# Optimization experiments

Measured on AMD Instinct MI355X. Metric: run time of the kernel, lower is better.

The kernel has to match this reference:

```python
import jax, jax.numpy as jnp
import numpy as np

HEAD_DIM = 64
N_HEADS = 64
N_KV = 8
Q_MULT = N_HEADS // N_KV  # 8
HIDDEN = 2880
SEQ = 1024
BATCH = 2
SLIDING_WINDOW = 128  # layer_idx=0 -> window active
ROPE_THETA = 150000.0
SCALING = 32.0
NTK_ALPHA = 1.0
NTK_BETA = 32.0
INIT_CTX = 4096
EPS = 1e-5


def _rope_caches(seq_len):
    # YaRN rotary caches (static numpy precompute, as in the source module)
    steps = np.arange(0, HEAD_DIM, 2, dtype=np.float32)
    freq = np.power(np.float32(ROPE_THETA), steps / np.float32(HEAD_DIM))
    concentration = np.float32(0.1) * np.log(np.float32(SCALING)) + 1.0
    d_half = np.float32(HEAD_DIM / 2.0)
    log_base = np.log(np.float32(ROPE_THETA))
    low = d_half * np.log(np.float32(INIT_CTX) / (np.float32(NTK_BETA) * np.float32(2.0 * np.pi))) / log_base
    high = d_half * np.log(np.float32(INIT_CTX) / (np.float32(NTK_ALPHA) * np.float32(2.0 * np.pi))) / log_base
    ramp = (np.arange(HEAD_DIM // 2, dtype=np.float32) - low) / (high - low)
    mask = 1.0 - np.clip(ramp, 0.0, 1.0)
    inv_freq = (1.0 / (np.float32(SCALING) * freq)) * (1.0 - mask) + (1.0 / freq) * mask
    pos = np.arange(seq_len, dtype=np.float32)
    freqs = np.einsum('i,j->ij', pos, inv_freq.astype(np.float32))
    cos = (np.cos(freqs) * concentration).astype(np.float32)
    sin = (np.sin(freqs) * concentration).astype(np.float32)
    return jnp.asarray(cos), jnp.asarray(sin)


def _apply_rotary(t, cos, sin):
    # t: (B, S, ..., head_dim); cos/sin: (S, head_dim//2). Rotate-half style.
    shape = (1, t.shape[1]) + (1,) * (t.ndim - 3) + (cos.shape[-1],)
    c = cos.reshape(shape)
    s = sin.reshape(shape)
    first, second = jnp.split(t, 2, axis=-1)
    return jnp.concatenate([first * c - second * s, second * c + first * s], axis=-1)


def setup_inputs() -> dict:
    key = jax.random.key(0)
    ks = jax.random.split(key, 6)
    qkv_dim = (N_HEADS + 2 * N_KV) * HEAD_DIM  # 5120
    return {
        'x': jax.random.normal(ks[0], (BATCH, SEQ, HIDDEN), dtype=jnp.float32),
        'norm_w': jnp.ones((HIDDEN,), dtype=jnp.float32),
        'qkv_w': jax.random.normal(ks[1], (qkv_dim, HIDDEN), dtype=jnp.float32) * 0.02,
        'qkv_b': jax.random.normal(ks[2], (qkv_dim,), dtype=jnp.float32) * 0.02,
        'out_w': jax.random.normal(ks[3], (HIDDEN, N_HEADS * HEAD_DIM), dtype=jnp.float32) * 0.02,
        'out_b': jax.random.normal(ks[4], (HIDDEN,), dtype=jnp.float32) * 0.02,
        'sinks': jax.random.normal(ks[5], (N_HEADS,), dtype=jnp.float32),
    }


def reference(x, norm_w, qkv_w, qkv_b, out_w, out_b, sinks):
    B, S, _ = x.shape
    # RMSNorm (fp32 accumulation)
    xf = x.astype(jnp.float32)
    rms = jnp.mean(xf * xf, axis=-1, keepdims=True)
    t = (xf * jax.lax.rsqrt(rms + EPS) * norm_w).astype(x.dtype)
    # QKV projection (fp32 accumulation)
    qkv = jnp.matmul(t.astype(jnp.float32), qkv_w.T) + qkv_b
    q_dim = N_HEADS * HEAD_DIM
    kv_dim = N_KV * HEAD_DIM
    q = qkv[..., :q_dim].reshape(B, S, N_KV, Q_MULT, HEAD_DIM)
    k = qkv[..., q_dim:q_dim + kv_dim].reshape(B, S, N_KV, HEAD_DIM)
    v = qkv[..., q_dim + kv_dim:].reshape(B, S, N_KV, HEAD_DIM)
    # YaRN rotary embedding
    cos, sin = _rope_caches(S)
    q = _apply_rotary(q, cos, sin)
    k = _apply_rotary(k, cos, sin)
    # causal + sliding-window mask
    neg_inf = jnp.float32(-jnp.inf)
    mask = jnp.triu(jnp.full((S, S), neg_inf, dtype=jnp.float32), k=1)
    mask = mask + jnp.tril(jnp.full((S, S), neg_inf, dtype=jnp.float32), k=-SLIDING_WINDOW)
    sm_scale = jnp.float32(1.0 / np.sqrt(HEAD_DIM))
    # GQA attention with sink logits
    logits = jnp.einsum('bqhmd,bkhd->bhmqk', q, k) * sm_scale + mask[None, None, None]
    sink = jnp.broadcast_to(sinks.reshape(1, N_KV, Q_MULT, 1, 1), (B, N_KV, Q_MULT, S, 1))
    logits = jnp.concatenate([logits, sink], axis=-1)
    w = jax.nn.softmax(logits, axis=-1)[..., :-1]  # drop sink column
    attn = jnp.einsum('bhmqk,bkhd->bqhmd', w, v).reshape(B, S, N_HEADS * HEAD_DIM)
    # output projection (fp32 accumulation) + residual
    out = jnp.matmul(attn, out_w.T) + out_b
    return x + out
```

## Files before the change

### kernel.cpp

```cpp
#include <hip/hip_runtime.h>

typedef unsigned short ushort_t;
typedef __attribute__((ext_vector_type(8))) short short8;
typedef __attribute__((ext_vector_type(8))) __bf16 bf16x8;
typedef __attribute__((ext_vector_type(4))) float float4v;
typedef __attribute__((ext_vector_type(4))) unsigned int uint4v;

__device__ __forceinline__ float bf2f(ushort_t u) {
    unsigned int v = ((unsigned int)u) << 16;
    return __builtin_bit_cast(float, v);
}
__device__ __forceinline__ ushort_t f2bf(float f) {
    unsigned int u = __builtin_bit_cast(unsigned int, f);
    unsigned int lsb = (u >> 16) & 1u;
    u += 0x7fffu + lsb;
    return (ushort_t)(u >> 16);
}
__device__ __forceinline__ uint4v pack8(const ushort_t* r) {
    uint4v u;
#pragma unroll
    for (int i = 0; i < 4; ++i)
        u[i] = (unsigned int)r[2 * i] | ((unsigned int)r[2 * i + 1] << 16);
    return u;
}
__device__ __forceinline__ void unpack8(uint4v u, float* f) {
#pragma unroll
    for (int i = 0; i < 4; ++i) {
        unsigned int x = u[i];
        f[2 * i] = __builtin_bit_cast(float, x << 16);
        f[2 * i + 1] = __builtin_bit_cast(float, x & 0xffff0000u);
    }
}
__device__ __forceinline__ uint4v ld8f32_bf(const float* p) {
    float4v a = *(const float4v*)p;
    float4v b = *(const float4v*)(p + 4);
    ushort_t r[8];
#pragma unroll
    for (int j = 0; j < 4; ++j) { r[j] = f2bf(a[j]); r[4 + j] = f2bf(b[j]); }
    return pack8(r);
}

#if __has_builtin(__builtin_amdgcn_global_load_lds)
#define HAVE_GLDS 1
__device__ __forceinline__ void glds16(const ushort_t* gp, ushort_t* lp) {
    __builtin_amdgcn_global_load_lds((const __attribute__((address_space(1))) void*)gp,
                                     (__attribute__((address_space(3))) void*)lp, 16, 0, 0);
}
#else
#define HAVE_GLDS 0
#endif

template <typename V>
__device__ __forceinline__ auto mfma_sel(V a, V b, float4v c, int)
    -> decltype(__builtin_amdgcn_mfma_f32_16x16x32_bf16(a, b, c, 0, 0, 0)) {
    return __builtin_amdgcn_mfma_f32_16x16x32_bf16(a, b, c, 0, 0, 0);
}
template <typename V>
__device__ __forceinline__ float4v mfma_sel(V a, V b, float4v c, long) {
    return __builtin_amdgcn_mfma_f32_16x16x32_bf16(__builtin_bit_cast(bf16x8, a),
                                                   __builtin_bit_cast(bf16x8, b), c, 0, 0, 0);
}
__device__ __forceinline__ float4v mfma_bf16(short8 a, short8 b, float4v c) {
    return mfma_sel(a, b, c, 0);
}

__device__ __forceinline__ float wave_sum(float v) {
#pragma unroll
    for (int o = 32; o; o >>= 1) v += __shfl_xor(v, o);
    return v;
}

#define HIDDEN 2880
#define NTOK 2048
#define QKV_DIM 5120
#define ATTN_DIM 4096
#define SM_SCALE 0.125f

__global__ __launch_bounds__(256) void f32_to_bf16_dual_kernel(const float* __restrict__ a,
                                                               ushort_t* __restrict__ ao, int na8,
                                                               const float* __restrict__ b,
                                                               ushort_t* __restrict__ bo, int nb8) {
    int idx = blockIdx.x * 256 + threadIdx.x;
    if (idx < na8) {
        *(uint4v*)(ao + (size_t)idx * 8) = ld8f32_bf(a + (size_t)idx * 8);
    } else {
        int j = idx - na8;
        if (j < nb8) *(uint4v*)(bo + (size_t)j * 8) = ld8f32_bf(b + (size_t)j * 8);
    }
}

__global__ __launch_bounds__(256) void rmsnorm_kernel(const float* __restrict__ x,
                                                      const float* __restrict__ wgt,
                                                      ushort_t* __restrict__ out) {
    const int tok = blockIdx.x, tid = threadIdx.x;
    const float* xr = x + (size_t)tok * HIDDEN;
    float v[16];
    float ss = 0.f;
#pragma unroll
    for (int i = 0; i < 2; ++i) {
        int c = tid + i * 256;
        if (c < 360) {
            float4v a = *(const float4v*)(xr + c * 8);
            float4v b = *(const float4v*)(xr + c * 8 + 4);
#pragma unroll
            for (int j = 0; j < 4; ++j) { v[i * 8 + j] = a[j]; v[i * 8 + 4 + j] = b[j]; }
#pragma unroll
            for (int j = 0; j < 8; ++j) ss += v[i * 8 + j] * v[i * 8 + j];
        }
    }
    ss = wave_sum(ss);
    __shared__ float red[4];
    if ((tid & 63) == 0) red[tid >> 6] = ss;
    __syncthreads();
    float scale = rsqrtf((red[0] + red[1] + red[2] + red[3]) * (1.f / 2880.f) + 1e-5f);
#pragma unroll
    for (int i = 0; i < 2; ++i) {
        int c = tid + i * 256;
        if (c < 360) {
            float4v wa = *(const float4v*)(wgt + c * 8);
            float4v wb = *(const float4v*)(wgt + c * 8 + 4);
            ushort_t r[8];
#pragma unroll
            for (int j = 0; j < 4; ++j) {
                r[j] = f2bf(v[i * 8 + j] * scale * wa[j]);
                r[4 + j] = f2bf(v[i * 8 + 4 + j] * scale * wb[j]);
            }
            *(uint4v*)(out + (size_t)tok * HIDDEN + c * 8) = pack8(r);
        }
    }
}

__global__ __launch_bounds__(256) void rope_apply_kernel(ushort_t* __restrict__ qkv) {
    int idx = blockIdx.x * 256 + threadIdx.x;
    int tok = idx / 288;
    int rem = idx - tok * 288;
    int h = rem >> 2, dg = rem & 3;
    int s = tok & 1023;
    size_t base = (size_t)tok * QKV_DIM + (h < 64 ? h * 64 : 4096 + (h - 64) * 64) + dg * 8;
    uint4v u1 = *(const uint4v*)(qkv + base);
    uint4v u2 = *(const uint4v*)(qkv + base + 32);
    float f1[8], f2[8];
    unpack8(u1, f1);
    unpack8(u2, f2);
    const float step = (float)(11.918390573078392 / 32.0);
    const float conc = (float)(1.3465735902799727);
    const float low = (float)(8.092890725542669);
    const float invden = (float)(1.0 / 9.305804387286162);
    ushort_t r1[8], r2[8];
#pragma unroll
    for (int jj = 0; jj < 8; ++jj) {
        int j = dg * 8 + jj;
        float invf = __expf(-(float)j * step);
        float ramp = ((float)j - low) * invden;
        float mask = 1.f - fminf(fmaxf(ramp, 0.f), 1.f);
        float inv_freq = invf * ((1.f - mask) * 0.03125f + mask);
        float ang = (float)s * inv_freq;
        float c = cosf(ang) * conc;
        float sn = sinf(ang) * conc;
        r1[jj] = f2bf(f1[jj] * c - f2[jj] * sn);
        r2[jj] = f2bf(f2[jj] * c + f1[jj] * sn);
    }
    *(uint4v*)(qkv + base) = pack8(r1);
    *(uint4v*)(qkv + base + 32) = pack8(r2);
}

template <int BN, bool RESID, bool OUTF32, bool BF16B>
__global__ __launch_bounds__(256) void gemm_kernel(const ushort_t* __restrict__ A,
                                                   const void* __restrict__ B,
                                                   const float* __restrict__ bias,
                                                   const float* __restrict__ resid,
                                                   void* __restrict__ Cout, int M, int N, int K) {
    constexpr int BM = 128, BK = 64;
    constexpr bool GL = BF16B && (HAVE_GLDS != 0);
    constexpr int LDT = GL ? 64 : 72;
    constexpr int NBUF = GL ? 2 : 1;
    static_assert(BN == 160 || BN == 128 || BN == 96 || BN == 64, "");
    __shared__ __align__(16) ushort_t As[NBUF][BM * LDT];
    __shared__ __align__(16) ushort_t Bs[NBUF][BN * LDT];

    const int m0 = blockIdx.y * BM;
    const int n0 = blockIdx.x * BN;
    const int tid = threadIdx.x;
    const int w = tid >> 6, lane = tid & 63;
    const int quad = lane >> 4, l16 = lane & 15;

    constexpr int WN = BN / 2;
    constexpr int NI = WN / 16;
    const int wm = (w >> 1) * 64;
    const int wn = (w & 1) * WN;

    float4v acc[4][NI];
#pragma unroll
    for (int i = 0; i < 4; ++i)
#pragma unroll
        for (int j = 0; j < NI; ++j) acc[i][j] = (float4v){0.f, 0.f, 0.f, 0.f};

    const int nk = K / BK;

#if HAVE_GLDS
    if constexpr (GL) {
        constexpr int NAI = BM / 32;
        constexpr int NBI = BN / 32;
        const ushort_t* Bp = (const ushort_t*)B;
        const ushort_t* agp[NAI];
        const ushort_t* bgp[NBI];
        ushort_t* alp[2][NAI];
        ushort_t* blp[2][NBI];
#pragma unroll
        for (int i = 0; i < NAI; ++i) {
            int sb = (w * NAI + i) * 64;
            int s = sb + lane, r = s >> 3, p = s & 7, c = p ^ (r & 7);
            agp[i] = A + (size_t)(m0 + r) * K + c * 8;
            alp[0][i] = &As[0][sb * 8];
            alp[1][i] = &As[1][sb * 8];
        }
#pragma unroll
        for (int i = 0; i < NBI; ++i) {
            int sb = (w * NBI + i) * 64;
            int s = sb + lane, r = s >> 3, p = s & 7, c = p ^ (r & 7);
            bgp[i] = Bp + (size_t)(n0 + r) * K + c * 8;
            blp[0][i] = &Bs[0][sb * 8];
            blp[1][i] = &Bs[1][sb * 8];
        }
#pragma unroll
        for (int i = 0; i < NAI; ++i) glds16(agp[i], alp[0][i]);
#pragma unroll
        for (int i = 0; i < NBI; ++i) glds16(bgp[i], blp[0][i]);
        __syncthreads();

        for (int kt = 0; kt < nk; ++kt) {
            const int cur = kt & 1;
            if (kt + 1 < nk) {
                const int k0 = (kt + 1) * BK;
#pragma unroll
                for (int i = 0; i < NAI; ++i) glds16(agp[i] + k0, alp[cur ^ 1][i]);
#pragma unroll
                for (int i = 0; i < NBI; ++i) glds16(bgp[i] + k0, blp[cur ^ 1][i]);
            }
            const ushort_t* Asb = As[cur];
            const ushort_t* Bsb = Bs[cur];
#pragma unroll
            for (int ks = 0; ks < 2; ++ks) {
                short8 af[4], bfr[NI];
#pragma unroll
                for (int mi = 0; mi < 4; ++mi) {
                    int row = wm + mi * 16 + l16;
                    af[mi] = *(const short8*)(Asb + row * LDT + ((ks * 4 + quad) ^ (row & 7)) * 8);
                }
#pragma unroll
                for (int ni = 0; ni < NI; ++ni) {
                    int row = wn + ni * 16 + l16;
                    bfr[ni] = *(const short8*)(Bsb + row * LDT + ((ks * 4 + quad) ^ (row & 7)) * 8);
                }
#pragma unroll
                for (int mi = 0; mi < 4; ++mi)
#pragma unroll
                    for (int ni = 0; ni < NI; ++ni)
                        acc[mi][ni] = mfma_bf16(af[mi], bfr[ni], acc[mi][ni]);
            }
            __syncthreads();
        }
    } else
#endif
    {
        constexpr int ACH = BM * BK / 8 / 256;
        constexpr int BCH = BN * BK / 8 / 256;
        uint4v areg[ACH], breg[BCH];
#pragma unroll
        for (int i = 0; i < ACH; ++i) {
            int c = tid + i * 256, r = c >> 3, col = c & 7;
            areg[i] = *(const uint4v*)(A + (size_t)(m0 + r) * K + col * 8);
        }
#pragma unroll
        for (int i = 0; i < BCH; ++i) {
            int c = tid + i * 256, r = c >> 3, col = c & 7;
            if constexpr (BF16B)
                breg[i] = *(const uint4v*)((const ushort_t*)B + (size_t)(n0 + r) * K + col * 8);
            else
                breg[i] = ld8f32_bf((const float*)B + (size_t)(n0 + r) * K + col * 8);
        }
        for (int kt = 0; kt < nk; ++kt) {
            __syncthreads();
#pragma unroll
            for (int i = 0; i < ACH; ++i) {
                int c = tid + i * 256, r = c >> 3, col = c & 7;
                *(uint4v*)(&As[0][r * LDT + col * 8]) = areg[i];
            }
#pragma unroll
            for (int i = 0; i < BCH; ++i) {
                int c = tid + i * 256, r = c >> 3, col = c & 7;
                *(uint4v*)(&Bs[0][r * LDT + col * 8]) = breg[i];
            }
            __syncthreads();
            if (kt + 1 < nk) {
                const int k0 = (kt + 1) * BK;
#pragma unroll
                for (int i = 0; i < ACH; ++i) {
                    int c = tid + i * 256, r = c >> 3, col = c & 7;
                    areg[i] = *(const uint4v*)(A + (size_t)(m0 + r) * K + k0 + col * 8);
                }
#pragma unroll
                for (int i = 0; i < BCH; ++i) {
                    int c = tid + i * 256, r = c >> 3, col = c & 7;
                    if constexpr (BF16B)
                        breg[i] = *(const uint4v*)((const ushort_t*)B + (size_t)(n0 + r) * K + k0 + col * 8);
                    else
                        breg[i] = ld8f32_bf((const float*)B + (size_t)(n0 + r) * K + k0 + col * 8);
                }
            }
#pragma unroll
            for (int ks = 0; ks < 2; ++ks) {
                short8 af[4], bfr[NI];
#pragma unroll
                for (int mi = 0; mi < 4; ++mi)
                    af[mi] = *(const short8*)(&As[0][(wm + mi * 16 + l16) * LDT + ks * 32 + quad * 8]);
#pragma unroll
                for (int ni = 0; ni < NI; ++ni)
                    bfr[ni] = *(const short8*)(&Bs[0][(wn + ni * 16 + l16) * LDT + ks * 32 + quad * 8]);
#pragma unroll
                for (int mi = 0; mi < 4; ++mi)
#pragma unroll
                    for (int ni = 0; ni < NI; ++ni)
                        acc[mi][ni] = mfma_bf16(af[mi], bfr[ni], acc[mi][ni]);
            }
        }
    }

#pragma unroll
    for (int ni = 0; ni < NI; ++ni) {
        int gc = n0 + wn + ni * 16 + l16;
        float bv = bias[gc];
#pragma unroll
        for (int mi = 0; mi < 4; ++mi) {
#pragma unroll
            for (int r = 0; r < 4; ++r) {
                int gr = m0 + wm + mi * 16 + quad * 4 + r;
                float vv = acc[mi][ni][r] + bv;
                if constexpr (RESID) vv += resid[(size_t)gr * N + gc];
                if constexpr (OUTF32) ((float*)Cout)[(size_t)gr * N + gc] = vv;
                else ((ushort_t*)Cout)[(size_t)gr * N + gc] = f2bf(vv);
            }
        }
    }
}

__global__ __launch_bounds__(256, 2) void attn_mfma_kernel(const ushort_t* __restrict__ qkv,
                                                           const float* __restrict__ sinks,
                                                           ushort_t* __restrict__ attnbuf) {
    constexpr int LDK = 72, LDV = 200, LDP = 200;
    __shared__ __align__(16) ushort_t Ks[192 * LDK];
    __shared__ __align__(16) ushort_t Vt[64 * LDV];
    __shared__ __align__(16) ushort_t Pb[4][16 * LDP];

    const int qc = blockIdx.x, kvh = blockIdx.y >> 1, half = blockIdx.y & 1, b = blockIdx.z;
    const int tid = threadIdx.x;
    const int w = tid >> 6, lane = tid & 63;
    const int quad = lane >> 4, l16 = lane & 15;
    const int w0 = qc * 64 - 127;

    for (int c = tid; c < 192 * 8; c += 256) {
        int row = c >> 3, col8 = c & 7;
        int pos = w0 + row;
        pos = pos < 0 ? 0 : (pos > 1023 ? 1023 : pos);
        size_t gk = ((size_t)(b * 1024 + pos)) * QKV_DIM + 4096 + kvh * 64 + col8 * 8;
        *(uint4v*)(Ks + row * LDK + col8 * 8) = *(const uint4v*)(qkv + gk);
        uint4v vv = *(const uint4v*)(qkv + gk + 512);
        ushort_t vs[8];
#pragma unroll
        for (int i = 0; i < 4; ++i) {
            vs[2 * i] = (ushort_t)(vv[i] & 0xffffu);
            vs[2 * i + 1] = (ushort_t)(vv[i] >> 16);
        }
#pragma unroll
        for (int j = 0; j < 8; ++j) Vt[(col8 * 8 + j) * LDV + row] = vs[j];
    }
    __syncthreads();

    short8 Vf[6][4];
#pragma unroll
    for (int kt = 0; kt < 6; ++kt)
#pragma unroll
        for (int nv = 0; nv < 4; ++nv)
            Vf[kt][nv] = *(const short8*)(Vt + (nv * 16 + l16) * LDV + kt * 32 + quad * 8);

    ushort_t* Pw = Pb[w];
    const int h = kvh * 8 + half * 4 + w;
    const float sink_f = sinks[h];

    for (int qtile = 0; qtile < 4; ++qtile) {
        const int tokb = b * 1024 + qc * 64 + qtile * 16;

        short8 qf[2];
        {
            const ushort_t* qp = qkv + ((size_t)(tokb + l16)) * QKV_DIM + h * 64 + quad * 8;
            qf[0] = *(const short8*)qp;
            qf[1] = *(const short8*)(qp + 32);
        }

        float4v acc[12];
#pragma unroll
        for (int nt = 0; nt < 12; ++nt) acc[nt] = (float4v){0.f, 0.f, 0.f, 0.f};
#pragma unroll
        for (int nt = 0; nt < 12; ++nt) {
#pragma unroll
            for (int ks = 0; ks < 2; ++ks) {
                short8 kf = *(const short8*)(Ks + (nt * 16 + l16) * LDK + ks * 32 + quad * 8);
                acc[nt] = mfma_bf16(qf[ks], kf, acc[nt]);
            }
        }

        float linv[4];
#pragma unroll
        for (int r = 0; r < 4; ++r) {
            const int ql = qtile * 16 + quad * 4 + r;
            float e[12];
            float mx = -1e30f;
#pragma unroll
            for (int nt = 0; nt < 12; ++nt) {
                int row_k = nt * 16 + l16;
                bool valid = (row_k >= ql) && (row_k <= ql + 127) && (w0 + row_k >= 0);
                float s = valid ? acc[nt][r] * SM_SCALE : -1e30f;
                e[nt] = s;
                mx = fmaxf(mx, s);
            }
#pragma unroll
            for (int o = 1; o < 16; o <<= 1) mx = fmaxf(mx, __shfl_xor(mx, o));
            float M = fmaxf(mx, sink_f);
            float ls = 0.f;
#pragma unroll
            for (int nt = 0; nt < 12; ++nt) {
                float ev = (e[nt] > -1e29f) ? __expf(e[nt] - M) : 0.f;
                e[nt] = ev;
                ls += ev;
            }
#pragma unroll
            for (int o = 1; o < 16; o <<= 1) ls += __shfl_xor(ls, o);
            linv[r] = 1.f / (ls + __expf(sink_f - M));
#pragma unroll
            for (int nt = 0; nt < 12; ++nt)
                Pw[(quad * 4 + r) * LDP + nt * 16 + l16] = f2bf(e[nt]);
        }

        float4v accO[4];
#pragma unroll
        for (int nv = 0; nv < 4; ++nv) accO[nv] = (float4v){0.f, 0.f, 0.f, 0.f};
#pragma unroll
        for (int kt = 0; kt < 6; ++kt) {
            short8 pf = *(const short8*)(Pw + l16 * LDP + kt * 32 + quad * 8);
#pragma unroll
            for (int nv = 0; nv < 4; ++nv) accO[nv] = mfma_bf16(pf, Vf[kt][nv], accO[nv]);
        }

#pragma unroll
        for (int r = 0; r < 4; ++r) {
            size_t ob = ((size_t)(tokb + quad * 4 + r)) * ATTN_DIM + h * 64 + l16;
#pragma unroll
            for (int nv = 0; nv < 4; ++nv)
                attnbuf[ob + nv * 16] = f2bf(accO[nv][r] * linv[r]);
        }
    }
}

extern "C" void kernel_launch(void* const* d_in, const int* in_sizes, int n_in,
                              void* d_out, int out_size, void* d_ws, size_t ws_size,
                              hipStream_t stream) {
    const float* x = (const float*)d_in[0];
    const float* norm_w = (const float*)d_in[1];
    const float* qkv_w = (const float*)d_in[2];
    const float* qkv_b = (const float*)d_in[3];
    const float* out_w = (const float*)d_in[4];
    const float* out_b = (const float*)d_in[5];
    const float* sinks = (const float*)d_in[6];
    float* outp = (float*)d_out;
    char* ws = (char*)d_ws;

    if (ws_size >= 86000000ull) {
        ushort_t* qkvbuf = (ushort_t*)ws;
        ushort_t* qkv_w_bf = (ushort_t*)(ws + 20971520);
        ushort_t* attnbuf = (ushort_t*)(ws + 20971520);
        ushort_t* Tbuf = (ushort_t*)(ws + 50462720);
        ushort_t* out_w_bf = (ushort_t*)(ws + 62259200);

        f32_to_bf16_dual_kernel<<<12960, 256, 0, stream>>>(qkv_w, qkv_w_bf, 1843200,
                                                           out_w, out_w_bf, 1474560);
        rmsnorm_kernel<<<NTOK, 256, 0, stream>>>(x, norm_w, Tbuf);
        gemm_kernel<160, false, false, true><<<dim3(32, 16), 256, 0, stream>>>(
            Tbuf, qkv_w_bf, qkv_b, nullptr, qkvbuf, NTOK, QKV_DIM, HIDDEN);
        rope_apply_kernel<<<2304, 256, 0, stream>>>(qkvbuf);
        attn_mfma_kernel<<<dim3(16, 16, 2), 256, 0, stream>>>(qkvbuf, sinks, attnbuf);
        gemm_kernel<96, true, true, true><<<dim3(30, 16), 256, 0, stream>>>(
            attnbuf, out_w_bf, out_b, x, outp, NTOK, HIDDEN, ATTN_DIM);
    } else {
        ushort_t* qkvbuf = (ushort_t*)ws;
        ushort_t* attnbuf = (ushort_t*)(ws + 20971520);
        ushort_t* Tbuf = (ushort_t*)d_out;

        rmsnorm_kernel<<<NTOK, 256, 0, stream>>>(x, norm_w, Tbuf);
        gemm_kernel<128, false, false, false><<<dim3(40, 16), 256, 0, stream>>>(
            Tbuf, qkv_w, qkv_b, nullptr, qkvbuf, NTOK, QKV_DIM, HIDDEN);
        rope_apply_kernel<<<2304, 256, 0, stream>>>(qkvbuf);
        attn_mfma_kernel<<<dim3(16, 16, 2), 256, 0, stream>>>(qkvbuf, sinks, attnbuf);
        gemm_kernel<96, true, true, false><<<dim3(30, 16), 256, 0, stream>>>(
            attnbuf, out_w, out_b, x, outp, NTOK, HIDDEN, ATTN_DIM);
    }
}
```

Before: 323.1 us.

## Skip masked key tiles in attention, remap GEMM workgroups across XCDs, reuse output buffer

The attention kernel now computes QK^T over only the 9 key tiles a query tile can reach in the sliding window instead of all 12. It runs the PV product over 5 k-steps instead of 6 and zeroes the one partially uncovered P tile. The GEMM kernels remap the workgroup index so consecutive blocks spread across the 8 XCDs for better L2 locality. The normalized-activation buffer moves into the output buffer, shrinking the workspace footprint. Risks are correctness of the tile-window arithmetic and the assumption that the grid size is divisible by 8.

```diff
diff --git a/kernel.cpp b/kernel.cpp
--- a/kernel.cpp
+++ b/kernel.cpp
@@ -178,8 +178,15 @@
     __shared__ __align__(16) ushort_t As[NBUF][BM * LDT];
     __shared__ __align__(16) ushort_t Bs[NBUF][BN * LDT];
 
-    const int m0 = blockIdx.y * BM;
-    const int n0 = blockIdx.x * BN;
+    const int nbx = gridDim.x;
+    int wg = blockIdx.y * nbx + blockIdx.x;
+    {
+        const int nwg = nbx * gridDim.y;
+        const int cpx = nwg >> 3;
+        wg = (wg & 7) * cpx + (wg >> 3);
+    }
+    const int m0 = (wg / nbx) * BM;
+    const int n0 = (wg % nbx) * BN;
     const int tid = threadIdx.x;
     const int w = tid >> 6, lane = tid & 63;
     const int quad = lane >> 4, l16 = lane & 15;
@@ -387,6 +394,7 @@
     const int h = kvh * 8 + half * 4 + w;
     const float sink_f = sinks[h];
 
+#pragma unroll
     for (int qtile = 0; qtile < 4; ++qtile) {
         const int tokb = b * 1024 + qc * 64 + qtile * 16;
 
@@ -397,30 +405,33 @@
             qf[1] = *(const short8*)(qp + 32);
         }
 
-        float4v acc[12];
-#pragma unroll
-        for (int nt = 0; nt < 12; ++nt) acc[nt] = (float4v){0.f, 0.f, 0.f, 0.f};
-#pragma unroll
-        for (int nt = 0; nt < 12; ++nt) {
+        float4v acc[9];
+#pragma unroll
+        for (int j = 0; j < 9; ++j) acc[j] = (float4v){0.f, 0.f, 0.f, 0.f};
+#pragma unroll
+        for (int j = 0; j < 9; ++j) {
+            const int nt = qtile + j;
 #pragma unroll
             for (int ks = 0; ks < 2; ++ks) {
                 short8 kf = *(const short8*)(Ks + (nt * 16 + l16) * LDK + ks * 32 + quad * 8);
-                acc[nt] = mfma_bf16(qf[ks], kf, acc[nt]);
-            }
-        }
+                acc[j] = mfma_bf16(qf[ks], kf, acc[j]);
+            }
+        }
+
+        const int ntz = (qtile & 1) ? (qtile - 1) : (qtile + 9);
 
         float linv[4];
 #pragma unroll
         for (int r = 0; r < 4; ++r) {
             const int ql = qtile * 16 + quad * 4 + r;
-            float e[12];
+            float e[9];
             float mx = -1e30f;
 #pragma unroll
-            for (int nt = 0; nt < 12; ++nt) {
-                int row_k = nt * 16 + l16;
+            for (int j = 0; j < 9; ++j) {
+                int row_k = (qtile + j) * 16 + l16;
                 bool valid = (row_k >= ql) && (row_k <= ql + 127) && (w0 + row_k >= 0);
-                float s = valid ? acc[nt][r] * SM_SCALE : -1e30f;
-                e[nt] = s;
+                float s = valid ? acc[j][r] * SM_SCALE : -1e30f;
+                e[j] = s;
                 mx = fmaxf(mx, s);
             }
 #pragma unroll
@@ -428,24 +439,26 @@
             float M = fmaxf(mx, sink_f);
             float ls = 0.f;
 #pragma unroll
-            for (int nt = 0; nt < 12; ++nt) {
-                float ev = (e[nt] > -1e29f) ? __expf(e[nt] - M) : 0.f;
-                e[nt] = ev;
+            for (int j = 0; j < 9; ++j) {
+                float ev = (e[j] > -1e29f) ? __expf(e[j] - M) : 0.f;
+                e[j] = ev;
                 ls += ev;
             }
 #pragma unroll
             for (int o = 1; o < 16; o <<= 1) ls += __shfl_xor(ls, o);
             linv[r] = 1.f / (ls + __expf(sink_f - M));
 #pragma unroll
-            for (int nt = 0; nt < 12; ++nt)
-                Pw[(quad * 4 + r) * LDP + nt * 16 + l16] = f2bf(e[nt]);
+            for (int j = 0; j < 9; ++j)
+                Pw[(quad * 4 + r) * LDP + (qtile + j) * 16 + l16] = f2bf(e[j]);
+            Pw[(quad * 4 + r) * LDP + ntz * 16 + l16] = 0;
         }
 
         float4v accO[4];
 #pragma unroll
         for (int nv = 0; nv < 4; ++nv) accO[nv] = (float4v){0.f, 0.f, 0.f, 0.f};
 #pragma unroll
-        for (int kt = 0; kt < 6; ++kt) {
+        for (int j = 0; j < 5; ++j) {
+            const int kt = (qtile >> 1) + j;
             short8 pf = *(const short8*)(Pw + l16 * LDP + kt * 32 + quad * 8);
 #pragma unroll
             for (int nv = 0; nv < 4; ++nv) accO[nv] = mfma_bf16(pf, Vf[kt][nv], accO[nv]);
@@ -478,8 +491,8 @@
         ushort_t* qkvbuf = (ushort_t*)ws;
         ushort_t* qkv_w_bf = (ushort_t*)(ws + 20971520);
         ushort_t* attnbuf = (ushort_t*)(ws + 20971520);
-        ushort_t* Tbuf = (ushort_t*)(ws + 50462720);
-        ushort_t* out_w_bf = (ushort_t*)(ws + 62259200);
+        ushort_t* out_w_bf = (ushort_t*)(ws + 50462720);
+        ushort_t* Tbuf = (ushort_t*)d_out;
 
         f32_to_bf16_dual_kernel<<<12960, 256, 0, stream>>>(qkv_w, qkv_w_bf, 1843200,
                                                            out_w, out_w_bf, 1474560);
```

New measurement: 316.8 us. No clear change (-1.9%).
